# Optimization experiments

Measured on AMD Instinct MI355X. Metric: run time of the kernel, lower is better.

The kernel has to match this reference:

```python
import jax, jax.numpy as jnp
import numpy as np

BASE = 10000.0

def _rope_neox(x, positions, head_dim):
    # x: [B, S, n_heads, head_dim]; positions: [B, S] int
    half = head_dim // 2
    inv_freq = 1.0 / (BASE ** (jnp.arange(0, head_dim, 2, dtype=jnp.float32) / head_dim))  # [half]
    freqs = positions.astype(jnp.float32)[..., None] * inv_freq  # [B, S, half]
    cos = jnp.cos(freqs)[:, :, None, :]  # [B, S, 1, half]
    sin = jnp.sin(freqs)[:, :, None, :]
    x1, x2 = x[..., :half], x[..., half:]
    return jnp.concatenate([x1 * cos - x2 * sin, x2 * cos + x1 * sin], axis=-1)

def setup_inputs() -> dict:
    key = jax.random.key(0)
    k1, k2, k3 = jax.random.split(key, 3)
    B, S, H = 1, 2048, 4096
    hidden_states = jax.random.normal(k1, (B, S, H), dtype=jnp.float32)
    position_ids = jnp.broadcast_to(jnp.arange(S, dtype=jnp.int32), (B, S))
    W_qkv = jax.random.normal(k2, (H, 3 * H), dtype=jnp.float32) * (H ** -0.5)
    W_o = jax.random.normal(k3, (H, H), dtype=jnp.float32) * (H ** -0.5)
    return {"hidden_states": hidden_states, "position_ids": position_ids, "W_qkv": W_qkv, "W_o": W_o}

def reference(hidden_states, position_ids, W_qkv, W_o):
    B, S, H = hidden_states.shape
    n_heads = 32
    head_dim = H // n_heads
    qkv = hidden_states @ W_qkv  # [B, S, 3H]
    q, k, v = jnp.split(qkv, 3, axis=-1)
    q = q.reshape(B, S, n_heads, head_dim)
    k = k.reshape(B, S, n_heads, head_dim)
    v = v.reshape(B, S, n_heads, head_dim)
    q = _rope_neox(q, position_ids, head_dim)
    k = _rope_neox(k, position_ids, head_dim)
    # causal SDPA (past_key_value=None -> is_causal=True)
    scale = 1.0 / jnp.sqrt(jnp.float32(head_dim))
    scores = jnp.einsum('bqhd,bkhd->bhqk', q, k) * scale  # [B, nH, S, S]
    causal = jnp.tril(jnp.ones((S, S), dtype=bool))
    scores = jnp.where(causal, scores, jnp.finfo(scores.dtype).min)
    probs = jax.nn.softmax(scores, axis=-1)
    attn = jnp.einsum('bhqk,bkhd->bqhd', probs, v).reshape(B, S, H)
    return attn @ W_o
```

## Files before the change

### kernel.cpp

```cpp
#include <hip/hip_runtime.h>
#include <hip/hip_bf16.h>
#include <math.h>

#define SEQ   2048
#define HID   4096
#define NHEAD 32
#define HD    128
#define QKVN  12288

typedef __bf16 bf16;
typedef __bf16 bf16x8 __attribute__((ext_vector_type(8)));
typedef __bf16 bf16x4 __attribute__((ext_vector_type(4)));
typedef float  f32x4  __attribute__((ext_vector_type(4)));

#define AS1 __attribute__((address_space(1)))
#define AS3 __attribute__((address_space(3)))

__device__ __forceinline__ void gload16(const void* g, void* l) {
    __builtin_amdgcn_global_load_lds((const AS1 void*)g, (AS3 void*)l, 16, 0, 0);
}

__device__ __forceinline__ unsigned short bbits(bf16 b) {
    union { bf16 b; unsigned short u; } x; x.b = b; return x.u;
}

__global__ __launch_bounds__(512) __attribute__((amdgpu_waves_per_eu(2, 2)))
void gemm256(const bf16* __restrict__ A, const bf16* __restrict__ Bt,
             bf16* __restrict__ C, int M, int N, int K) {
    __shared__ __attribute__((aligned(16))) char lds[131072];
    const int tid  = threadIdx.x;
    const int l    = tid & 63;
    const int wave = tid >> 6;
    const int wr   = wave >> 2;
    const int wc   = wave & 3;
    const int lh   = l >> 4;
    const int ll   = l & 15;
    const int by   = blockIdx.x & 7, bx = blockIdx.x >> 3;
    const int brow = by * 256, bcol = bx * 256;

    f32x4 acc[4][4][2];
    #pragma unroll
    for (int q = 0; q < 4; ++q)
        #pragma unroll
        for (int f = 0; f < 4; ++f)
            #pragma unroll
            for (int g = 0; g < 2; ++g) acc[q][f][g] = (f32x4){0.f, 0.f, 0.f, 0.f};

    const int trow = tid >> 3, tslot = tid & 7;
    const int srcs = (tslot ^ (trow & 7)) * 16;
    const size_t rowb = (size_t)K * 2;
    const char* pA[2][2]; const char* pB[2][2];
    #pragma unroll
    for (int h = 0; h < 2; ++h)
        #pragma unroll
        for (int i = 0; i < 2; ++i) {
            pA[h][i] = (const char*)A  + (size_t)(brow + h*128 + i*64 + trow) * rowb + srcs;
            pB[h][i] = (const char*)Bt + (size_t)(bcol + h*128 + i*64 + trow) * rowb + srcs;
        }

#define SA(buf, h) do { \
        gload16(pA[h][0], lds + (buf)*65536 + (h)*16384 + tid*16); \
        gload16(pA[h][1], lds + (buf)*65536 + (h)*16384 + 8192 + tid*16); \
        pA[h][0] += 128; pA[h][1] += 128; \
    } while (0)
#define SB(buf, h) do { \
        gload16(pB[h][0], lds + (buf)*65536 + 32768 + (h)*16384 + tid*16); \
        gload16(pB[h][1], lds + (buf)*65536 + 32768 + (h)*16384 + 8192 + tid*16); \
        pB[h][0] += 128; pB[h][1] += 128; \
    } while (0)

    const int sw0 = ((0 + lh) ^ (ll & 7)) << 4;
    const int sw1 = ((4 + lh) ^ (ll & 7)) << 4;

    bf16x8 af[4][2], bv0[2][2], bv1[2][2];

#define LOADA(Xb, mh) do { \
        const char* LA_ = lds + (Xb)*65536 + (mh)*16384 + (wr*64 + ll)*128; \
        _Pragma("unroll") \
        for (int f_ = 0; f_ < 4; ++f_) { \
            af[f_][0] = *(const bf16x8*)(LA_ + f_*2048 + sw0); \
            af[f_][1] = *(const bf16x8*)(LA_ + f_*2048 + sw1); \
        } \
    } while (0)
#define LOADB(Xb, nh, bvv) do { \
        const char* LB_ = lds + (Xb)*65536 + 32768 + (nh)*16384 + (wc*32 + ll)*128; \
        _Pragma("unroll") \
        for (int g_ = 0; g_ < 2; ++g_) { \
            bvv[g_][0] = *(const bf16x8*)(LB_ + g_*2048 + sw0); \
            bvv[g_][1] = *(const bf16x8*)(LB_ + g_*2048 + sw1); \
        } \
    } while (0)
#define FENCE_MMA(WAITSTR, q, bvv) do { \
        asm volatile(WAITSTR ::: "memory"); \
        __builtin_amdgcn_s_barrier(); \
        asm volatile("s_waitcnt lgkmcnt(0)" ::: "memory"); \
        __builtin_amdgcn_sched_barrier(0); \
        __builtin_amdgcn_s_setprio(1); \
        _Pragma("unroll") \
        for (int f_ = 0; f_ < 4; ++f_) \
            _Pragma("unroll") \
            for (int g_ = 0; g_ < 2; ++g_) { \
                acc[q][f_][g_] = __builtin_amdgcn_mfma_f32_16x16x32_bf16( \
                    af[f_][0], bvv[g_][0], acc[q][f_][g_], 0, 0, 0); \
                acc[q][f_][g_] = __builtin_amdgcn_mfma_f32_16x16x32_bf16( \
                    af[f_][1], bvv[g_][1], acc[q][f_][g_], 0, 0, 0); \
            } \
        __builtin_amdgcn_s_setprio(0); \
        __builtin_amdgcn_s_barrier(); \
    } while (0)

    SA(0, 0); SB(0, 0); SB(0, 1); SA(0, 1); SA(1, 0); SB(1, 0);
    asm volatile("s_waitcnt vmcnt(8)" ::: "memory");
    __builtin_amdgcn_s_barrier();

    const int NT = K >> 6;
    for (int u = 0; u < NT - 1; ++u) {
        const int X = u & 1, Y = X ^ 1;
        LOADA(X, 0); LOADB(X, 0, bv0); SB(Y, 1);
        FENCE_MMA("s_waitcnt vmcnt(8)", 0, bv0);
        LOADB(X, 1, bv1); SA(Y, 1);
        FENCE_MMA("s_waitcnt vmcnt(8)", 1, bv1);
        LOADA(X, 1);
        if (u < NT - 2) { SA(X, 0); }
        FENCE_MMA("s_waitcnt vmcnt(8)", 2, bv0);
        if (u < NT - 2) { SB(X, 0); }
        FENCE_MMA("s_waitcnt vmcnt(8)", 3, bv1);
    }
    {
        const int X = (NT - 1) & 1;
        LOADA(X, 0); LOADB(X, 0, bv0);
        FENCE_MMA("s_waitcnt vmcnt(4)", 0, bv0);
        LOADB(X, 1, bv1);
        FENCE_MMA("s_waitcnt vmcnt(2)", 1, bv1);
        LOADA(X, 1);
        FENCE_MMA("s_waitcnt vmcnt(0)", 2, bv0);
        FENCE_MMA("s_nop 0", 3, bv1);
    }
#undef FENCE_MMA
#undef LOADA
#undef LOADB
#undef SA
#undef SB

    __syncthreads();
    float* ep = (float*)lds + wave * 2304;
    const int c8 = (l & 3) * 8;
    #pragma unroll
    for (int q = 0; q < 4; ++q) {
        const int mh = q >> 1, nh = q & 1;
        #pragma unroll
        for (int f = 0; f < 4; ++f)
            #pragma unroll
            for (int g = 0; g < 2; ++g)
                #pragma unroll
                for (int j = 0; j < 4; ++j)
                    ep[(f*16 + lh*4 + j) * 36 + g*16 + ll] = acc[q][f][g][j];
        #pragma unroll
        for (int it = 0; it < 4; ++it) {
            int r2 = it * 16 + (l >> 2);
            const float* src = ep + r2 * 36 + c8;
            bf16x8 o;
            #pragma unroll
            for (int j = 0; j < 8; ++j) o[j] = (bf16)src[j];
            size_t grow = (size_t)(brow + mh*128 + wr*64 + r2);
            *(bf16x8*)(C + grow * N + bcol + nh*128 + wc*32 + c8) = o;
        }
    }
}

template<int OB>
__global__ __launch_bounds__(512, 2) void gemm2p(const bf16* __restrict__ A,
                                                 const bf16* __restrict__ Bt,
                                                 void* __restrict__ Cv,
                                                 int M, int N, int K) {
    __shared__ __attribute__((aligned(16))) char lds[98304];
    const int tid  = threadIdx.x;
    const int l    = tid & 63;
    const int wave = tid >> 6;
    const int wr   = wave >> 2;
    const int wc   = wave & 3;
    const int lh   = l >> 4;
    const int ll   = l & 15;

    const int by   = blockIdx.x & 7;
    const int bx   = blockIdx.x >> 3;
    const int brow = by * 256, bcol = bx * 128;

    f32x4 acc[2][4][2];
    #pragma unroll
    for (int m = 0; m < 2; ++m)
        #pragma unroll
        for (int f = 0; f < 4; ++f)
            #pragma unroll
            for (int g = 0; g < 2; ++g) acc[m][f][g] = (f32x4){0.f, 0.f, 0.f, 0.f};

    const int trow = tid >> 3, tslot = tid & 7;
    const int srcs = (tslot ^ (trow & 7)) * 16;
    const size_t rowb = (size_t)K * 2;
    const char* pA[2][2]; const char* pB[2];
    #pragma unroll
    for (int h = 0; h < 2; ++h)
        #pragma unroll
        for (int i = 0; i < 2; ++i)
            pA[h][i] = (const char*)A + (size_t)(brow + h*128 + i*64 + trow) * rowb + srcs;
    #pragma unroll
    for (int i = 0; i < 2; ++i)
        pB[i] = (const char*)Bt + (size_t)(bcol + i*64 + trow) * rowb + srcs;

#define SA(buf, h) do { \
        gload16(pA[h][0], lds + (buf)*32768 + (h)*16384 + tid*16); \
        gload16(pA[h][1], lds + (buf)*32768 + (h)*16384 + 8192 + tid*16); \
        pA[h][0] += 128; pA[h][1] += 128; \
    } while (0)
#define SB(buf) do { \
        gload16(pB[0], lds + 65536 + (buf)*16384 + tid*16); \
        gload16(pB[1], lds + 65536 + (buf)*16384 + 8192 + tid*16); \
        pB[0] += 128; pB[1] += 128; \
    } while (0)

    const int sw0 = ((0 + lh) ^ (ll & 7)) << 4;
    const int sw1 = ((4 + lh) ^ (ll & 7)) << 4;

#define PHASE(Xb, mh, STAGE_STMT, WAITSTR) do { \
        const char* LA_ = lds + (Xb)*32768 + (mh)*16384 + (wr*64 + ll)*128; \
        const char* LB_ = lds + 65536 + (Xb)*16384 + (wc*32 + ll)*128; \
        bf16x8 af_[4][2], bv_[2][2]; \
        _Pragma("unroll") \
        for (int f_ = 0; f_ < 4; ++f_) { \
            af_[f_][0] = *(const bf16x8*)(LA_ + f_*2048 + sw0); \
            af_[f_][1] = *(const bf16x8*)(LA_ + f_*2048 + sw1); \
        } \
        _Pragma("unroll") \
        for (int g_ = 0; g_ < 2; ++g_) { \
            bv_[g_][0] = *(const bf16x8*)(LB_ + g_*2048 + sw0); \
            bv_[g_][1] = *(const bf16x8*)(LB_ + g_*2048 + sw1); \
        } \
        STAGE_STMT; \
        asm volatile(WAITSTR ::: "memory"); \
        __builtin_amdgcn_s_barrier(); \
        asm volatile("s_waitcnt lgkmcnt(0)" ::: "memory"); \
        __builtin_amdgcn_sched_barrier(0); \
        __builtin_amdgcn_s_setprio(1); \
        _Pragma("unroll") \
        for (int f_ = 0; f_ < 4; ++f_) \
            _Pragma("unroll") \
            for (int g_ = 0; g_ < 2; ++g_) { \
                acc[mh][f_][g_] = __builtin_amdgcn_mfma_f32_16x16x32_bf16( \
                    af_[f_][0], bv_[g_][0], acc[mh][f_][g_], 0, 0, 0); \
                acc[mh][f_][g_] = __builtin_amdgcn_mfma_f32_16x16x32_bf16( \
                    af_[f_][1], bv_[g_][1], acc[mh][f_][g_], 0, 0, 0); \
            } \
        __builtin_amdgcn_s_setprio(0); \
        __builtin_amdgcn_s_barrier(); \
    } while (0)

    SA(0, 0); SB(0); SA(0, 1); SA(1, 0);
    asm volatile("s_waitcnt vmcnt(4)" ::: "memory");
    __builtin_amdgcn_s_barrier();

    const int NT = K >> 6;
    for (int u = 0; u < NT - 2; ++u) {
        const int X = u & 1, Y = X ^ 1;
        PHASE(X, 0, SB(Y), "s_waitcnt vmcnt(4)");
        PHASE(X, 1, { SA(Y, 1); SA(X, 0); }, "s_waitcnt vmcnt(4)");
    }
    {
        const int X = (NT - 2) & 1, Y = X ^ 1;
        PHASE(X, 0, SB(Y), "s_waitcnt vmcnt(4)");
        PHASE(X, 1, SA(Y, 1), "s_waitcnt vmcnt(2)");
    }
    {
        const int X = (NT - 1) & 1;
        PHASE(X, 0, ((void)0), "s_waitcnt vmcnt(0)");
        PHASE(X, 1, ((void)0), "s_nop 0");
    }
#undef PHASE
#undef SA
#undef SB

    __syncthreads();
    float* ep = (float*)lds + wave * 2304;
    const int cq = l & 3;
    #pragma unroll
    for (int mh = 0; mh < 2; ++mh) {
        #pragma unroll
        for (int f = 0; f < 4; ++f)
            #pragma unroll
            for (int g = 0; g < 2; ++g)
                #pragma unroll
                for (int j = 0; j < 4; ++j)
                    ep[(f*16 + lh*4 + j) * 36 + g*16 + ll] = acc[mh][f][g][j];
        #pragma unroll
        for (int it = 0; it < 4; ++it) {
            int r2 = it * 16 + (l >> 2);
            const float* src = ep + r2 * 36 + cq * 8;
            size_t grow = (size_t)(brow + mh*128 + wr*64 + r2);
            int gcol = bcol + wc*32 + cq*8;
            if (OB == 0) {
                float* dst = (float*)Cv + grow * N + gcol;
                *(f32x4*)dst       = *(const f32x4*)src;
                *(f32x4*)(dst + 4) = *(const f32x4*)(src + 4);
            } else {
                bf16x8 o;
                #pragma unroll
                for (int jj = 0; jj < 8; ++jj) o[jj] = (bf16)src[jj];
                *(bf16x8*)((bf16*)Cv + grow * N + gcol) = o;
            }
        }
    }
}

__global__ __launch_bounds__(256) void cast_flat(const float* __restrict__ in,
                                                 bf16* __restrict__ out, int n8) {
    int i = blockIdx.x * 256 + threadIdx.x;
    if (i >= n8) return;
    float4 a = ((const float4*)in)[2 * i];
    float4 b = ((const float4*)in)[2 * i + 1];
    bf16x8 o = {(bf16)a.x, (bf16)a.y, (bf16)a.z, (bf16)a.w,
                (bf16)b.x, (bf16)b.y, (bf16)b.z, (bf16)b.w};
    *(bf16x8*)(out + (size_t)i * 8) = o;
}

__global__ __launch_bounds__(256) void cast_transpose(const float* __restrict__ in,
                                                      bf16* __restrict__ out, int R, int C) {
    __shared__ float t[64][65];
    const int r0 = blockIdx.y * 64, c0 = blockIdx.x * 64;
    #pragma unroll
    for (int i = 0; i < 4; ++i) {
        int idx = i * 256 + threadIdx.x;
        int rr = idx >> 4, c4 = (idx & 15) * 4;
        float4 v = *(const float4*)&in[(size_t)(r0 + rr) * C + c0 + c4];
        t[rr][c4] = v.x; t[rr][c4 + 1] = v.y; t[rr][c4 + 2] = v.z; t[rr][c4 + 3] = v.w;
    }
    __syncthreads();
    #pragma unroll
    for (int i = 0; i < 2; ++i) {
        int idx = i * 256 + threadIdx.x;
        int rr = idx >> 3, c8 = (idx & 7) * 8;
        bf16x8 o;
        #pragma unroll
        for (int j = 0; j < 8; ++j) o[j] = (bf16)t[c8 + j][rr];
        *(bf16x8*)&out[(size_t)(c0 + rr) * R + r0 + c8] = o;
    }
}

__global__ __launch_bounds__(256) void rope_table(const int* __restrict__ pos_ids,
                                                  float2* __restrict__ tab) {
    int id = blockIdx.x * 256 + threadIdx.x;
    int s = id >> 6, d = id & 63;
    float pos = (float)pos_ids[s];
    float inv = expf(-9.210340371976184f * ((float)d * (1.0f / 64.0f)));
    float sn, cs;
    sincosf(pos * inv, &sn, &cs);
    tab[id] = make_float2(cs, sn);
}

__global__ __launch_bounds__(256) void rope_repack(const bf16* __restrict__ qkv,
                                                   const float2* __restrict__ tab,
                                                   bf16* __restrict__ Qb,
                                                   bf16* __restrict__ Kb) {
    int id = blockIdx.x * 256 + threadIdx.x;
    const int d4 = (id & 15) * 4;
    const int h  = (id >> 4) & (NHEAD - 1);
    const int s  = id >> 9;

    float2 tr[4];
    #pragma unroll
    for (int i = 0; i < 4; ++i) tr[i] = tab[s * 64 + d4 + i];

    const bf16* row = qkv + (size_t)s * QKVN;
    {
        bf16x4 lo = *(const bf16x4*)(row + h * HD + d4);
        bf16x4 hi = *(const bf16x4*)(row + h * HD + 64 + d4);
        bf16x4 olo, ohi;
        #pragma unroll
        for (int i = 0; i < 4; ++i) {
            float x1 = (float)lo[i], x2 = (float)hi[i];
            olo[i] = (bf16)(x1 * tr[i].x - x2 * tr[i].y);
            ohi[i] = (bf16)(x2 * tr[i].x + x1 * tr[i].y);
        }
        bf16* qo = Qb + ((size_t)h * SEQ + s) * HD;
        *(bf16x4*)(qo + d4) = olo;
        *(bf16x4*)(qo + 64 + d4) = ohi;
    }
    {
        bf16x4 lo = *(const bf16x4*)(row + HID + h * HD + d4);
        bf16x4 hi = *(const bf16x4*)(row + HID + h * HD + 64 + d4);
        bf16x4 olo, ohi;
        #pragma unroll
        for (int i = 0; i < 4; ++i) {
            float x1 = (float)lo[i], x2 = (float)hi[i];
            olo[i] = (bf16)(x1 * tr[i].x - x2 * tr[i].y);
            ohi[i] = (bf16)(x2 * tr[i].x + x1 * tr[i].y);
        }
        bf16* ko = Kb + ((size_t)h * SEQ + s) * HD;
        *(bf16x4*)(ko + d4) = olo;
        *(bf16x4*)(ko + 64 + d4) = ohi;
    }
}

__global__ __launch_bounds__(256) void v_transpose(const bf16* __restrict__ qkv,
                                                   bf16* __restrict__ Vt) {
    __shared__ bf16 t[64][130];
    const int h = blockIdx.y, s0 = blockIdx.x * 64;
    #pragma unroll
    for (int i = 0; i < 4; ++i) {
        int idx = i * 256 + threadIdx.x;
        int ss = idx >> 4, c8 = (idx & 15) * 8;
        bf16x8 v = *(const bf16x8*)&qkv[(size_t)(s0 + ss) * QKVN + 2 * HID + h * HD + c8];
        #pragma unroll
        for (int j = 0; j < 8; ++j) t[ss][c8 + j] = v[j];
    }
    __syncthreads();
    #pragma unroll
    for (int i = 0; i < 4; ++i) {
        int idx = i * 256 + threadIdx.x;
        int dd = idx >> 3, s8 = (idx & 7) * 8;
        bf16x8 o;
        #pragma unroll
        for (int j = 0; j < 8; ++j) o[j] = t[s8 + j][dd];
        *(bf16x8*)&Vt[((size_t)h * HD + dd) * SEQ + s0 + s8] = o;
    }
}

__global__ __launch_bounds__(256) void attn_mfma(const bf16* __restrict__ Qb,
                                                 const bf16* __restrict__ Kb,
                                                 const bf16* __restrict__ Vt,
                                                 bf16* __restrict__ attn) {
    __shared__ __attribute__((aligned(16))) char Ka[2][16384];
    __shared__ __attribute__((aligned(16))) char Va[2][16384];
    __shared__ __attribute__((aligned(16))) char Ps[4 * 2048];
    const int tid  = threadIdx.x, l = tid & 63, wave = tid >> 6;
    const int head = blockIdx.x;
    const int qb   = gridDim.y - 1 - blockIdx.y;
    const int q0   = qb * 64;
    const int qw   = q0 + wave * 16;
    const float scale = 0.08838834764831845f;

    bf16x8 qf[4];
    const bf16* Qg = Qb + ((size_t)head * SEQ + qw + (l & 15)) * HD;
    #pragma unroll
    for (int kc = 0; kc < 4; ++kc) qf[kc] = *(const bf16x8*)(Qg + kc * 32 + (l >> 4) * 8);

    f32x4 o[8];
    #pragma unroll
    for (int i = 0; i < 8; ++i) o[i] = (f32x4){0.f, 0.f, 0.f, 0.f};
    float mrun = -1e30f, lrun = 0.f;
    const int qrow  = qw + (l & 15);
    const int ntile = qb + 1;

    const char* Kg = (const char*)(Kb + (size_t)head * SEQ * HD);
    const char* Vg = (const char*)(Vt + (size_t)head * HD * SEQ);
    char* Pw = Ps + wave * 2048;

#define ASTAGE(b, t0) do { \
        const int kv0_ = (t0) * 64; \
        _Pragma("unroll") \
        for (int i = 0; i < 4; ++i) { \
            int c = i * 256 + tid; \
            int rk_ = c >> 4, slk_ = c & 15; \
            gload16(Kg + (size_t)(kv0_ + rk_) * 256 + ((slk_ * 16) ^ ((rk_ & 15) << 4)), \
                    Ka[b] + (size_t)(i * 256 + (tid & 192)) * 16); \
            int rv_ = c >> 3, slv_ = c & 7; \
            gload16(Vg + (size_t)rv_ * (SEQ * 2) + (size_t)kv0_ * 2 + ((slv_ * 16) ^ ((rv_ & 7) << 4)), \
                    Va[b] + (size_t)(i * 256 + (tid & 192)) * 16); \
        } \
    } while (0)

    ASTAGE(0, 0);
    asm volatile("s_waitcnt vmcnt(0)" ::: "memory");
    __builtin_amdgcn_s_barrier();

    for (int t = 0; t < ntile; ++t) {
        const int cur = t & 1;
        const int kv0 = t * 64;
        if (t + 1 < ntile) ASTAGE(cur ^ 1, t + 1);

        f32x4 st[4];
        __builtin_amdgcn_s_setprio(1);
        #pragma unroll
        for (int mf = 0; mf < 4; ++mf) {
            f32x4 s = (f32x4){0.f, 0.f, 0.f, 0.f};
            #pragma unroll
            for (int kc = 0; kc < 4; ++kc) {
                int rk = mf * 16 + (l & 15);
                bf16x8 a = *(const bf16x8*)(Ka[cur] + rk * 256 +
                              ((kc * 64 + (l >> 4) * 16) ^ ((rk & 15) << 4)));
                s = __builtin_amdgcn_mfma_f32_16x16x32_bf16(a, qf[kc], s, 0, 0, 0);
            }
            st[mf] = s;
        }
        __builtin_amdgcn_s_setprio(0);

        float pm = -1e30f;
        #pragma unroll
        for (int mf = 0; mf < 4; ++mf)
            #pragma unroll
            for (int j = 0; j < 4; ++j) {
                int kv = kv0 + mf * 16 + (l >> 4) * 4 + j;
                float v = (kv <= qrow) ? st[mf][j] * scale : -1e30f;
                st[mf][j] = v;
                pm = fmaxf(pm, v);
            }
        pm = fmaxf(pm, __shfl_xor(pm, 16));
        pm = fmaxf(pm, __shfl_xor(pm, 32));
        float mn   = fmaxf(mrun, pm);
        float corr = __expf(mrun - mn);
        float ls = 0.f;
        #pragma unroll
        for (int mf = 0; mf < 4; ++mf)
            #pragma unroll
            for (int j = 0; j < 4; ++j) {
                float p = __expf(st[mf][j] - mn);
                st[mf][j] = p;
                ls += p;
            }
        ls += __shfl_xor(ls, 16);
        ls += __shfl_xor(ls, 32);
        lrun = lrun * corr + ls;
        mrun = mn;

        f32x4 cv;
        #pragma unroll
        for (int r = 0; r < 4; ++r) cv[r] = __shfl(corr, (l >> 4) * 4 + r, 64);
        #pragma unroll
        for (int nf = 0; nf < 8; ++nf) o[nf] *= cv;

        #pragma unroll
        for (int mf = 0; mf < 4; ++mf)
            #pragma unroll
            for (int r = 0; r < 4; r += 2) {
                int kv = mf * 16 + (l >> 4) * 4 + r;
                unsigned pk = (unsigned)bbits((bf16)st[mf][r]) |
                              ((unsigned)bbits((bf16)st[mf][r + 1]) << 16);
                *(unsigned*)(Pw + (l & 15) * 128 + ((kv * 2) ^ ((l & 15 & 7) << 4))) = pk;
            }

        __builtin_amdgcn_s_setprio(1);
        #pragma unroll
        for (int kc = 0; kc < 2; ++kc) {
            bf16x8 pa = *(const bf16x8*)(Pw + (l & 15) * 128 +
                           ((kc * 64 + (l >> 4) * 16) ^ ((l & 7) << 4)));
            #pragma unroll
            for (int nf = 0; nf < 8; ++nf) {
                int dr = nf * 16 + (l & 15);
                bf16x8 vb = *(const bf16x8*)(Va[cur] + dr * 128 +
                               ((kc * 64 + (l >> 4) * 16) ^ ((dr & 7) << 4)));
                o[nf] = __builtin_amdgcn_mfma_f32_16x16x32_bf16(pa, vb, o[nf], 0, 0, 0);
            }
        }
        __builtin_amdgcn_s_setprio(0);

        asm volatile("s_waitcnt vmcnt(0) lgkmcnt(0)" ::: "memory");
        __builtin_amdgcn_s_barrier();
    }
#undef ASTAGE

    float il = 1.0f / lrun;
    f32x4 iv;
    #pragma unroll
    for (int r = 0; r < 4; ++r) iv[r] = __shfl(il, (l >> 4) * 4 + r, 64);
    #pragma unroll
    for (int nf = 0; nf < 8; ++nf)
        #pragma unroll
        for (int r = 0; r < 4; ++r) {
            int row = qw + (l >> 4) * 4 + r;
            attn[(size_t)row * HID + head * HD + nf * 16 + (l & 15)] = (bf16)(o[nf][r] * iv[r]);
        }
}

extern "C" void kernel_launch(void* const* d_in, const int* in_sizes, int n_in,
                              void* d_out, int out_size, void* d_ws, size_t ws_size,
                              hipStream_t stream) {
    const float* hidden  = (const float*)d_in[0];
    const int*   pos_ids = (const int*)d_in[1];
    const float* W_qkv   = (const float*)d_in[2];
    const float* W_o     = (const float*)d_in[3];
    float*       out     = (float*)d_out;
    char*        ws      = (char*)d_ws;

    bf16*   Wqkv_t   = (bf16*)(ws);
    bf16*   qkv_b    = (bf16*)(ws + 100663296);
    bf16*   hidden_b = (bf16*)(ws + 150994944);
    float2* tab      = (float2*)(ws + 150994944);
    bf16* Qb     = (bf16*)(ws);
    bf16* Kb     = (bf16*)(ws + 16777216);
    bf16* Vtb    = (bf16*)(ws + 33554432);
    bf16* attn_b = (bf16*)(ws + 50331648);
    bf16* Wo_t   = (bf16*)(ws + 67108864);

    cast_flat<<<SEQ * HID / 8 / 256, 256, 0, stream>>>(hidden, hidden_b, SEQ * HID / 8);
    cast_transpose<<<dim3(QKVN / 64, HID / 64), 256, 0, stream>>>(W_qkv, Wqkv_t, HID, QKVN);
    gemm256<<<(QKVN / 256) * (SEQ / 256), 512, 0, stream>>>(hidden_b, Wqkv_t, qkv_b,
                                                            SEQ, QKVN, HID);
    rope_table<<<SEQ * 64 / 256, 256, 0, stream>>>(pos_ids, tab);
    rope_repack<<<SEQ * NHEAD * 16 / 256, 256, 0, stream>>>(qkv_b, tab, Qb, Kb);
    v_transpose<<<dim3(SEQ / 64, NHEAD), 256, 0, stream>>>(qkv_b, Vtb);
    cast_transpose<<<dim3(HID / 64, HID / 64), 256, 0, stream>>>(W_o, Wo_t, HID, HID);
    attn_mfma<<<dim3(NHEAD, SEQ / 64), 256, 0, stream>>>(Qb, Kb, Vtb, attn_b);
    gemm2p<0><<<(HID / 128) * (SEQ / 256), 512, 0, stream>>>(attn_b, Wo_t, out,
                                                             SEQ, HID, HID);
}
```

Baseline: 458.9 us.

## Retile QKV GEMM to 256x192 blocks with restructured double-buffered pipeline

Changes the QKV projection GEMM tile from 256x256 to 256x192, which gives 512 blocks instead of 384. The likely aim is better wave quantization across the CUs (384 blocks is 1.5 waves on 256 CUs, 512 is exactly 2). The K-loop is rewritten to two MFMA phases per 64-wide K step, with whole-tile A/B staging into double buffers, and the epilogue now writes bf16x4 stores per 16-row fragment. The smaller N tile lowers arithmetic intensity, and the shallower prefetch may expose more memory latency.

```diff
diff --git a/kernel.cpp b/kernel.cpp
--- a/kernel.cpp
+++ b/kernel.cpp
@@ -25,9 +25,9 @@
 }
 
 __global__ __launch_bounds__(512) __attribute__((amdgpu_waves_per_eu(2, 2)))
-void gemm256(const bf16* __restrict__ A, const bf16* __restrict__ Bt,
+void gemm192(const bf16* __restrict__ A, const bf16* __restrict__ Bt,
              bf16* __restrict__ C, int M, int N, int K) {
-    __shared__ __attribute__((aligned(16))) char lds[131072];
+    __shared__ __attribute__((aligned(16))) char lds[114688];
     const int tid  = threadIdx.x;
     const int l    = tid & 63;
     const int wave = tid >> 6;
@@ -36,61 +36,56 @@
     const int lh   = l >> 4;
     const int ll   = l & 15;
     const int by   = blockIdx.x & 7, bx = blockIdx.x >> 3;
-    const int brow = by * 256, bcol = bx * 256;
-
-    f32x4 acc[4][4][2];
-    #pragma unroll
-    for (int q = 0; q < 4; ++q)
+    const int brow = by * 256, bcol = bx * 192;
+
+    f32x4 acc[2][4][3];
+    #pragma unroll
+    for (int m = 0; m < 2; ++m)
         #pragma unroll
         for (int f = 0; f < 4; ++f)
             #pragma unroll
-            for (int g = 0; g < 2; ++g) acc[q][f][g] = (f32x4){0.f, 0.f, 0.f, 0.f};
+            for (int g = 0; g < 3; ++g) acc[m][f][g] = (f32x4){0.f, 0.f, 0.f, 0.f};
 
     const int trow = tid >> 3, tslot = tid & 7;
     const int srcs = (tslot ^ (trow & 7)) * 16;
     const size_t rowb = (size_t)K * 2;
-    const char* pA[2][2]; const char* pB[2][2];
-    #pragma unroll
-    for (int h = 0; h < 2; ++h)
-        #pragma unroll
-        for (int i = 0; i < 2; ++i) {
-            pA[h][i] = (const char*)A  + (size_t)(brow + h*128 + i*64 + trow) * rowb + srcs;
-            pB[h][i] = (const char*)Bt + (size_t)(bcol + h*128 + i*64 + trow) * rowb + srcs;
-        }
-
-#define SA(buf, h) do { \
-        gload16(pA[h][0], lds + (buf)*65536 + (h)*16384 + tid*16); \
-        gload16(pA[h][1], lds + (buf)*65536 + (h)*16384 + 8192 + tid*16); \
-        pA[h][0] += 128; pA[h][1] += 128; \
-    } while (0)
-#define SB(buf, h) do { \
-        gload16(pB[h][0], lds + (buf)*65536 + 32768 + (h)*16384 + tid*16); \
-        gload16(pB[h][1], lds + (buf)*65536 + 32768 + (h)*16384 + 8192 + tid*16); \
-        pB[h][0] += 128; pB[h][1] += 128; \
+    const char* pA[4]; const char* pB[3];
+    #pragma unroll
+    for (int i = 0; i < 4; ++i)
+        pA[i] = (const char*)A + (size_t)(brow + i*64 + trow) * rowb + srcs;
+    #pragma unroll
+    for (int i = 0; i < 3; ++i)
+        pB[i] = (const char*)Bt + (size_t)(bcol + i*64 + trow) * rowb + srcs;
+
+#define SAU(buf, i) do { \
+        gload16(pA[i], lds + (buf)*32768 + (i)*8192 + tid*16); pA[i] += 128; \
+    } while (0)
+#define SBU(buf, i) do { \
+        gload16(pB[i], lds + 65536 + (buf)*24576 + (i)*8192 + tid*16); pB[i] += 128; \
     } while (0)
 
     const int sw0 = ((0 + lh) ^ (ll & 7)) << 4;
     const int sw1 = ((4 + lh) ^ (ll & 7)) << 4;
 
-    bf16x8 af[4][2], bv0[2][2], bv1[2][2];
+    bf16x8 af[4][2], bv[3][2];
 
 #define LOADA(Xb, mh) do { \
-        const char* LA_ = lds + (Xb)*65536 + (mh)*16384 + (wr*64 + ll)*128; \
+        const char* LA_ = lds + (Xb)*32768 + ((mh)*128 + wr*64 + ll)*128; \
         _Pragma("unroll") \
         for (int f_ = 0; f_ < 4; ++f_) { \
             af[f_][0] = *(const bf16x8*)(LA_ + f_*2048 + sw0); \
             af[f_][1] = *(const bf16x8*)(LA_ + f_*2048 + sw1); \
         } \
     } while (0)
-#define LOADB(Xb, nh, bvv) do { \
-        const char* LB_ = lds + (Xb)*65536 + 32768 + (nh)*16384 + (wc*32 + ll)*128; \
-        _Pragma("unroll") \
-        for (int g_ = 0; g_ < 2; ++g_) { \
-            bvv[g_][0] = *(const bf16x8*)(LB_ + g_*2048 + sw0); \
-            bvv[g_][1] = *(const bf16x8*)(LB_ + g_*2048 + sw1); \
+#define LOADB(Xb) do { \
+        const char* LB_ = lds + 65536 + (Xb)*24576 + (wc*48 + ll)*128; \
+        _Pragma("unroll") \
+        for (int g_ = 0; g_ < 3; ++g_) { \
+            bv[g_][0] = *(const bf16x8*)(LB_ + g_*2048 + sw0); \
+            bv[g_][1] = *(const bf16x8*)(LB_ + g_*2048 + sw1); \
         } \
     } while (0)
-#define FENCE_MMA(WAITSTR, q, bvv) do { \
+#define FENCE_MMA(WAITSTR, mh) do { \
         asm volatile(WAITSTR ::: "memory"); \
         __builtin_amdgcn_s_barrier(); \
         asm volatile("s_waitcnt lgkmcnt(0)" ::: "memory"); \
@@ -99,71 +94,64 @@
         _Pragma("unroll") \
         for (int f_ = 0; f_ < 4; ++f_) \
             _Pragma("unroll") \
-            for (int g_ = 0; g_ < 2; ++g_) { \
-                acc[q][f_][g_] = __builtin_amdgcn_mfma_f32_16x16x32_bf16( \
-                    af[f_][0], bvv[g_][0], acc[q][f_][g_], 0, 0, 0); \
-                acc[q][f_][g_] = __builtin_amdgcn_mfma_f32_16x16x32_bf16( \
-                    af[f_][1], bvv[g_][1], acc[q][f_][g_], 0, 0, 0); \
+            for (int g_ = 0; g_ < 3; ++g_) { \
+                acc[mh][f_][g_] = __builtin_amdgcn_mfma_f32_16x16x32_bf16( \
+                    af[f_][0], bv[g_][0], acc[mh][f_][g_], 0, 0, 0); \
+                acc[mh][f_][g_] = __builtin_amdgcn_mfma_f32_16x16x32_bf16( \
+                    af[f_][1], bv[g_][1], acc[mh][f_][g_], 0, 0, 0); \
             } \
         __builtin_amdgcn_s_setprio(0); \
         __builtin_amdgcn_s_barrier(); \
     } while (0)
 
-    SA(0, 0); SB(0, 0); SB(0, 1); SA(0, 1); SA(1, 0); SB(1, 0);
-    asm volatile("s_waitcnt vmcnt(8)" ::: "memory");
+    SBU(0, 0); SBU(0, 1); SBU(0, 2);
+    SAU(0, 0); SAU(0, 1); SAU(0, 2); SAU(0, 3);
+    asm volatile("s_waitcnt vmcnt(2)" ::: "memory");
     __builtin_amdgcn_s_barrier();
 
     const int NT = K >> 6;
     for (int u = 0; u < NT - 1; ++u) {
         const int X = u & 1, Y = X ^ 1;
-        LOADA(X, 0); LOADB(X, 0, bv0); SB(Y, 1);
-        FENCE_MMA("s_waitcnt vmcnt(8)", 0, bv0);
-        LOADB(X, 1, bv1); SA(Y, 1);
-        FENCE_MMA("s_waitcnt vmcnt(8)", 1, bv1);
+        LOADA(X, 0); LOADB(X);
+        SBU(Y, 0); SBU(Y, 1); SBU(Y, 2);
+        FENCE_MMA("s_waitcnt vmcnt(3)", 0);
         LOADA(X, 1);
-        if (u < NT - 2) { SA(X, 0); }
-        FENCE_MMA("s_waitcnt vmcnt(8)", 2, bv0);
-        if (u < NT - 2) { SB(X, 0); }
-        FENCE_MMA("s_waitcnt vmcnt(8)", 3, bv1);
+        SAU(Y, 0); SAU(Y, 1); SAU(Y, 2); SAU(Y, 3);
+        FENCE_MMA("s_waitcnt vmcnt(2)", 1);
     }
     {
         const int X = (NT - 1) & 1;
-        LOADA(X, 0); LOADB(X, 0, bv0);
-        FENCE_MMA("s_waitcnt vmcnt(4)", 0, bv0);
-        LOADB(X, 1, bv1);
-        FENCE_MMA("s_waitcnt vmcnt(2)", 1, bv1);
+        LOADA(X, 0); LOADB(X);
+        FENCE_MMA("s_waitcnt vmcnt(0)", 0);
         LOADA(X, 1);
-        FENCE_MMA("s_waitcnt vmcnt(0)", 2, bv0);
-        FENCE_MMA("s_nop 0", 3, bv1);
+        FENCE_MMA("s_nop 0", 1);
     }
 #undef FENCE_MMA
 #undef LOADA
 #undef LOADB
-#undef SA
-#undef SB
+#undef SAU
+#undef SBU
 
     __syncthreads();
-    float* ep = (float*)lds + wave * 2304;
-    const int c8 = (l & 3) * 8;
-    #pragma unroll
-    for (int q = 0; q < 4; ++q) {
-        const int mh = q >> 1, nh = q & 1;
-        #pragma unroll
-        for (int f = 0; f < 4; ++f)
-            #pragma unroll
-            for (int g = 0; g < 2; ++g)
+    float* ep = (float*)lds + wave * (16 * 52);
+    #pragma unroll
+    for (int mh = 0; mh < 2; ++mh) {
+        #pragma unroll
+        for (int f = 0; f < 4; ++f) {
+            #pragma unroll
+            for (int g = 0; g < 3; ++g)
                 #pragma unroll
                 for (int j = 0; j < 4; ++j)
-                    ep[(f*16 + lh*4 + j) * 36 + g*16 + ll] = acc[q][f][g][j];
-        #pragma unroll
-        for (int it = 0; it < 4; ++it) {
-            int r2 = it * 16 + (l >> 2);
-            const float* src = ep + r2 * 36 + c8;
-            bf16x8 o;
-            #pragma unroll
-            for (int j = 0; j < 8; ++j) o[j] = (bf16)src[j];
-            size_t grow = (size_t)(brow + mh*128 + wr*64 + r2);
-            *(bf16x8*)(C + grow * N + bcol + nh*128 + wc*32 + c8) = o;
+                    ep[(lh*4 + j) * 52 + g*16 + ll] = acc[mh][f][g][j];
+            #pragma unroll
+            for (int it = 0; it < 3; ++it) {
+                int row = l >> 2;
+                int c4  = (l & 3) + it * 4;
+                const float* src = ep + row * 52 + c4 * 4;
+                bf16x4 o = {(bf16)src[0], (bf16)src[1], (bf16)src[2], (bf16)src[3]};
+                size_t grow = (size_t)(brow + mh*128 + wr*64 + f*16 + row);
+                *(bf16x4*)(C + grow * N + bcol + wc*48 + c4*4) = o;
+            }
         }
     }
 }
@@ -591,7 +579,7 @@
 
     cast_flat<<<SEQ * HID / 8 / 256, 256, 0, stream>>>(hidden, hidden_b, SEQ * HID / 8);
     cast_transpose<<<dim3(QKVN / 64, HID / 64), 256, 0, stream>>>(W_qkv, Wqkv_t, HID, QKVN);
-    gemm256<<<(QKVN / 256) * (SEQ / 256), 512, 0, stream>>>(hidden_b, Wqkv_t, qkv_b,
+    gemm192<<<(QKVN / 192) * (SEQ / 256), 512, 0, stream>>>(hidden_b, Wqkv_t, qkv_b,
                                                             SEQ, QKVN, HID);
     rope_table<<<SEQ * 64 / 256, 256, 0, stream>>>(pos_ids, tab);
     rope_repack<<<SEQ * NHEAD * 16 / 256, 256, 0, stream>>>(qkv_b, tab, Qb, Kb);
```

Result: slower. 486.2 us (+6.0%).
